# Kernel optimization log

Hardware: AMD Instinct MI355X
Metric: run time of the kernel (lower is better)

## Reference

```python
import jax, jax.numpy as jnp
import numpy as np

NUM_BANDS = 30
NUM_CH = 128
DIFF_HEAD_DIM = NUM_CH // 4 // 2  # 16
GRAPH_HEADS = 4
GRAPH_HD = NUM_CH // GRAPH_HEADS  # 32
SCALES = [2, 4, 8, 16, 32]


def _band_config():
    widths = np.array([2,3,3,3,3,3,3,3,3,3,3,8,8,8,8,8,8,8,8,8,8,8,8,16,16,16,16,16,16,16,17], dtype=np.float64)
    starts = np.concatenate([[0.0], np.cumsum(widths)])[:NUM_BANDS]
    freqs = (starts + widths[:NUM_BANDS] / 2.0) * 31.25
    slot = {2: 0, 4: 1, 8: 2, 16: 3, 32: 4}
    scale_slots, init_w = [], []
    for f in freqs:
        if f < 500:
            sc, iw = [8, 16, 32], [0.1, 0.3, 0.6]
        elif f < 2000:
            sc, iw = [4, 8, 16], [0.3, 0.4, 0.3]
        else:
            sc, iw = [2, 4, 8], [0.6, 0.3, 0.1]
        scale_slots.append([slot[s] for s in sc])
        init_w.append(iw)
    return freqs, np.array(scale_slots, np.int32), np.array(init_w, np.float32)

BAND_FREQS, SCALE_SLOTS, INIT_W = _band_config()


def setup_inputs() -> dict:
    key = jax.random.key(0)
    ks = iter(jax.random.split(key, 64))
    B, N, T, K = 4, NUM_CH, 512, NUM_BANDS

    def nrm(shape, fan):
        return jax.random.normal(next(ks), shape, jnp.float32) / np.sqrt(fan)

    inp = {}
    inp['x'] = jax.random.normal(next(ks), (B, N, T, K), jnp.float32)
    # per-band differential attention weights (stored [in, out])
    inp['Wq'] = nrm((K, N, N), N)
    inp['Wk'] = nrm((K, N, N), N)
    inp['Wv'] = nrm((K, N, N // 2), N)
    inp['Wo'] = nrm((K, N // 2, N), N // 2)
    inp['bo'] = jnp.zeros((K, N), jnp.float32)
    # per-band lambda predictors
    inp['lw1'] = nrm((K, 8, 16), 8)
    inp['lb1'] = jnp.zeros((K, 16), jnp.float32)
    inp['lw2'] = nrm((K, 16, 1), 16)
    inp['lb2'] = jnp.zeros((K, 1), jnp.float32)
    # shared multiscale conv kernels (torch OIH layout)
    for s in SCALES:
        inp[f'cw{s}'] = nrm((N, N, s), N * s)
        inp[f'cb{s}'] = jnp.zeros((N,), jnp.float32)
    inp['fusion_w'] = jnp.asarray(INIT_W)
    inp['band_embed'] = jnp.log(jnp.asarray(BAND_FREQS, jnp.float32) + 1.0)[:, None] * jax.random.normal(next(ks), (K, 64), jnp.float32) * 0.1
    # graph attention weights
    inp['gWq'] = nrm((N, N), N); inp['gbq'] = jnp.zeros((N,), jnp.float32)
    inp['gWk'] = nrm((N, N), N); inp['gbk'] = jnp.zeros((N,), jnp.float32)
    inp['gWv'] = nrm((N, N), N); inp['gbv'] = jnp.zeros((N,), jnp.float32)
    inp['gWo'] = nrm((N, N), N); inp['gbo'] = jnp.zeros((N,), jnp.float32)
    return inp


def reference(x, Wq, Wk, Wv, Wo, bo, lw1, lb1, lw2, lb2,
              cw2, cb2, cw4, cb4, cw8, cb8, cw16, cb16, cw32, cb32,
              fusion_w, band_embed, gWq, gbq, gWk, gbk, gWv, gbv, gWo, gbo):
    B, N, T, K = x.shape

    # ---- 1. Differential band attention (vectorized over the 30 bands) ----
    xb = jnp.transpose(x, (3, 0, 2, 1))                         # [K,B,T,N]
    q = jnp.einsum('kbtn,knm->kbtm', xb, Wq)
    kk = jnp.einsum('kbtn,knm->kbtm', xb, Wk)
    v = jnp.einsum('kbtn,knd->kbtd', xb, Wv)                    # [K,B,T,N/2]
    q1, q2 = jnp.split(q, 2, axis=-1)
    k1, k2 = jnp.split(kk, 2, axis=-1)
    inv = 1.0 / np.sqrt(DIFF_HEAD_DIM)
    a1 = jax.nn.softmax(jnp.einsum('kbtd,kbsd->kbts', q1, k1) * inv, axis=-1)
    a2 = jax.nn.softmax(jnp.einsum('kbtd,kbsd->kbts', q2, k2) * inv, axis=-1)

    def stats(a):  # mean / unbiased std / max / min over the [T,T] map
        return (a.mean(axis=(-2, -1)), jnp.std(a, axis=(-2, -1), ddof=1),
                a.max(axis=(-2, -1)), a.min(axis=(-2, -1)))

    st = jnp.stack(stats(a1) + stats(a2), axis=-1)              # [K,B,8]
    h = jax.nn.relu(jnp.einsum('kbi,kio->kbo', st, lw1) + lb1[:, None, :])
    lam = jax.nn.sigmoid(jnp.einsum('kbo,koj->kbj', h, lw2) + lb2[:, None, :])[..., None]  # [K,B,1,1]
    ad = a1 - lam * a2
    ob = jnp.einsum('kbts,kbsd->kbtd', ad, v)
    ob = jnp.einsum('kbtd,kdn->kbtn', ob, Wo) + bo[:, None, None, :]
    h1 = jnp.transpose(ob, (1, 3, 2, 0))                        # [B,N,T,K]

    # ---- 2. Frequency-adaptive multiscale conv fusion ----
    xm = jnp.transpose(h1, (0, 3, 1, 2)).reshape(B * K, N, T)   # bands into batch

    def conv(xc, w, b, s):
        y = jax.lax.conv_general_dilated(xc, w, (1,), [(s // 2, s // 2)],
                                         dimension_numbers=('NCH', 'OIH', 'NCH'))
        return y[:, :, :T] + b[None, :, None]                   # trim even-kernel extra frame

    co = jnp.stack([conv(xm, w, b, s) for (w, b, s) in
                    [(cw2, cb2, 2), (cw4, cb4, 4), (cw8, cb8, 8), (cw16, cb16, 16), (cw32, cb32, 32)]], 0)
    sw = jax.nn.softmax(fusion_w, axis=-1)                      # [K,3]
    Wfull = jnp.zeros((K, 5), x.dtype).at[jnp.arange(K)[:, None], jnp.asarray(SCALE_SLOTS)].set(sw)
    co = co.reshape(5, B, K, N, T)
    h2 = jnp.transpose(jnp.einsum('ks,sbknt->bknt', Wfull, co), (0, 2, 3, 1))  # [B,N,T,K]

    # ---- 3. Learnable harmonic graph attention across bands ----
    e = band_embed / (jnp.linalg.norm(band_embed, axis=-1, keepdims=True) + 1e-8)
    sim = e @ e.T
    vals, idx = jax.lax.top_k(sim, 5)
    A = jnp.zeros((K, K), x.dtype).at[jnp.arange(K)[:, None], idx].set(vals)
    A = (A + A.T) / 2
    M = B * T
    xg = jnp.transpose(h2, (0, 2, 3, 1)).reshape(M, K, N)       # [B*T, 30, 128]
    qg = jnp.transpose((xg @ gWq + gbq).reshape(M, K, GRAPH_HEADS, GRAPH_HD), (0, 2, 1, 3))
    kg = jnp.transpose((xg @ gWk + gbk).reshape(M, K, GRAPH_HEADS, GRAPH_HD), (0, 2, 1, 3))
    vg = jnp.transpose((xg @ gWv + gbv).reshape(M, K, GRAPH_HEADS, GRAPH_HD), (0, 2, 1, 3))
    sc = jnp.einsum('mhid,mhjd->mhij', qg, kg) / np.sqrt(float(GRAPH_HD))
    sc = jnp.where((A != 0)[None, None], sc, -jnp.inf)
    at = jnp.nan_to_num(jax.nn.softmax(sc, axis=-1))
    og = jnp.einsum('mhij,mhjd->mhid', at, vg)
    og = jnp.transpose(og, (0, 2, 1, 3)).reshape(M, K, N) @ gWo + gbo
    out = jnp.transpose(og.reshape(B, T, K, N), (0, 3, 1, 2))   # [B,N,T,K]
    return out
```

## Files before the change

kernel.cpp:

```cpp
#include <hip/hip_runtime.h>

typedef const float* fp;
typedef unsigned short u16;
typedef __attribute__((ext_vector_type(8))) short bf16x8;
typedef __attribute__((ext_vector_type(4))) float f32x4;

__device__ __forceinline__ u16 f2b(float f) {
  union { float f; unsigned u; } a; a.f = f;
  unsigned u = a.u;
  u += 0x7fffu + ((u >> 16) & 1u);
  return (u16)(u >> 16);
}
__device__ __forceinline__ void splitf(float x, u16& h, u16& l) {
  union { float f; unsigned u; } a; a.f = x;
  unsigned hu = a.u & 0xFFFF0000u;
  h = (u16)(hu >> 16);
  union { unsigned u; float f; } b; b.u = hu;
  l = f2b(x - b.f);
}

__global__ __launch_bounds__(64) void k_adj(fp be, float* mask) {
  __shared__ float e[30][65];
  __shared__ float sim[30][33];
  __shared__ float A[30][33];
  int tid = threadIdx.x;
  for (int idx = tid; idx < 30 * 64; idx += 64) e[idx / 64][idx % 64] = be[idx];
  __syncthreads();
  if (tid < 30) {
    float s = 0.f;
    for (int d = 0; d < 64; d++) s += e[tid][d] * e[tid][d];
    float sc = 1.0f / (sqrtf(s) + 1e-8f);
    for (int d = 0; d < 64; d++) e[tid][d] *= sc;
  }
  __syncthreads();
  if (tid < 30) {
    for (int j = 0; j < 30; j++) {
      float s = 0.f;
      for (int d = 0; d < 64; d++) s += e[tid][d] * e[j][d];
      sim[tid][j] = s;
    }
    for (int j = 0; j < 30; j++) A[tid][j] = 0.f;
  }
  __syncthreads();
  if (tid < 30) {
    unsigned used = 0;
    for (int t = 0; t < 5; t++) {
      float best = -1e30f; int bi = 0;
      for (int j = 0; j < 30; j++)
        if (!((used >> j) & 1u) && sim[tid][j] > best) { best = sim[tid][j]; bi = j; }
      A[tid][bi] = best; used |= 1u << bi;
    }
  }
  __syncthreads();
  for (int idx = tid; idx < 900; idx += 64) {
    int i = idx / 30, j = idx % 30;
    float s = A[i][j] + A[j][i];
    mask[idx] = (s != 0.0f) ? 1.0f : 0.0f;
  }
}

__global__ __launch_bounds__(256) void k_wt_band(fp Wq, fp Wk, fp Wv, u16* wh, u16* wl) {
  int kb = blockIdx.x, which = blockIdx.y;
  __shared__ float wsb[128][129];
  int tid = threadIdx.x;
  int M = (which == 2) ? 64 : 128;
  int sh = (which == 2) ? 6 : 7;
  fp src = (which == 0) ? (Wq + kb * 16384) : (which == 1) ? (Wk + kb * 16384) : (Wv + kb * 8192);
  for (int i = tid; i < 128 * M; i += 256) {
    int n = i >> sh, m = i & (M - 1);
    wsb[n][m] = src[i];
  }
  __syncthreads();
  long base = (long)kb * 40960 + which * 16384;
  for (int o = tid; o < 128 * M; o += 256) {
    int m = o >> 7, n = o & 127;
    u16 h, l; splitf(wsb[n][m], h, l);
    wh[base + m * 128 + n] = h; wl[base + m * 128 + n] = l;
  }
}

__global__ __launch_bounds__(256) void k_wt_graph(fp gWq, fp gWk, fp gWv, fp gWo,
                                                  u16* wh, u16* wl) {
  int w = blockIdx.x;
  fp src = (w == 0) ? gWq : (w == 1) ? gWk : (w == 2) ? gWv : gWo;
  __shared__ float wsb[128][129];
  int tid = threadIdx.x;
  for (int i = tid; i < 16384; i += 256) wsb[i >> 7][i & 127] = src[i];
  __syncthreads();
  long base = (long)w * 16384;
  for (int o = tid; o < 16384; o += 256) {
    int m = o >> 7, n = o & 127;
    u16 h, l; splitf(wsb[n][m], h, l);
    wh[base + m * 128 + n] = h; wl[base + m * 128 + n] = l;
  }
}

__global__ __launch_bounds__(256) void k_qkv(fp x, const u16* wh, const u16* wl,
                                             u16* qh, u16* ql, u16* kh, u16* kl,
                                             u16* vTh, u16* vTl) {
  int kb = blockIdx.z, b = blockIdx.y, t0 = blockIdx.x * 64;
  int tid = threadIdx.x;
  int wave = tid >> 6, lane = tid & 63, l15 = lane & 15, quad = lane >> 4;
  __shared__ u16 xs_h[64 * 136];
  __shared__ u16 xs_l[64 * 136];
  for (int i = tid; i < 8192; i += 256) {
    int tl = i >> 7, n = i & 127;
    float v = x[((long)(b * 128 + n) * 512 + t0 + tl) * 30 + kb];
    u16 h, l; splitf(v, h, l);
    xs_h[tl * 136 + n] = h; xs_l[tl * 136 + n] = l;
  }
  __syncthreads();
  int arow = wave * 16 + l15;
  bf16x8 Ah[4], Al[4];
#pragma unroll
  for (int kc = 0; kc < 4; kc++) {
    Ah[kc] = *(const bf16x8*)(xs_h + arow * 136 + kc * 32 + quad * 8);
    Al[kc] = *(const bf16x8*)(xs_l + arow * 136 + kc * 32 + quad * 8);
  }
  int pair = kb * 4 + b;
  const u16* wbh = wh + (long)kb * 40960;
  const u16* wbl = wl + (long)kb * 40960;
  for (int c = 0; c < 20; c++) {
    f32x4 d = {0.f, 0.f, 0.f, 0.f};
#pragma unroll
    for (int kc = 0; kc < 4; kc++) {
      long boff = (long)(c * 16 + l15) * 128 + kc * 32 + quad * 8;
      bf16x8 Bh = *(const bf16x8*)(wbh + boff);
      bf16x8 Bl = *(const bf16x8*)(wbl + boff);
      d = __builtin_amdgcn_mfma_f32_16x16x32_bf16(Ah[kc], Bh, d, 0, 0, 0);
      d = __builtin_amdgcn_mfma_f32_16x16x32_bf16(Ah[kc], Bl, d, 0, 0, 0);
      d = __builtin_amdgcn_mfma_f32_16x16x32_bf16(Al[kc], Bh, d, 0, 0, 0);
    }
    if (c < 8) {
      int m = c * 16 + l15;
#pragma unroll
      for (int r = 0; r < 4; r++) {
        int trow = t0 + wave * 16 + quad * 4 + r;
        u16 h, l; splitf(d[r], h, l);
        long o = ((long)pair * 512 + trow) * 128 + m;
        qh[o] = h; ql[o] = l;
      }
    } else if (c < 16) {
      int m = (c - 8) * 16 + l15;
#pragma unroll
      for (int r = 0; r < 4; r++) {
        int trow = t0 + wave * 16 + quad * 4 + r;
        u16 h, l; splitf(d[r], h, l);
        long o = ((long)pair * 512 + trow) * 128 + m;
        kh[o] = h; kl[o] = l;
      }
    } else {
      int dcol = (c - 16) * 16 + l15;
#pragma unroll
      for (int r = 0; r < 4; r++) {
        int trow = t0 + wave * 16 + quad * 4 + r;
        u16 h, l; splitf(d[r], h, l);
        long o = ((long)pair * 64 + dcol) * 512 + trow;
        vTh[o] = h; vTl[o] = l;
      }
    }
  }
}

__global__ __launch_bounds__(256) void k_flash(const u16* qh, const u16* ql,
                                               const u16* kh, const u16* kl,
                                               const u16* vTh, const u16* vTl,
                                               float* rowstats, float* ob1, float* ob2) {
  int pair = blockIdx.y;
  int t0 = blockIdx.x * 16;
  int tid = threadIdx.x;
  int wave = tid >> 6, lane = tid & 63;
  int l15 = lane & 15, quad = lane >> 4;

  __shared__ float fbig[8704];
  __shared__ float st[2][16][4][4];
  __shared__ float fin[2][16][2];

  const long pb = (long)pair * 512 * 128;
  const u16* qhb = qh + pb; const u16* qlb = ql + pb;
  const u16* khb = kh + pb; const u16* klb = kl + pb;

  float sc[2][8][4];
  float mw[2][4];
#pragma unroll
  for (int h = 0; h < 2; h++) {
    long abase = (long)(t0 + l15) * 128 + h * 64 + quad * 8;
    bf16x8 Ah0 = *(const bf16x8*)(qhb + abase);
    bf16x8 Ah1 = *(const bf16x8*)(qhb + abase + 32);
    bf16x8 Al0 = *(const bf16x8*)(qlb + abase);
    bf16x8 Al1 = *(const bf16x8*)(qlb + abase + 32);
#pragma unroll
    for (int ct = 0; ct < 8; ct++) {
      int scol = wave * 128 + ct * 16 + l15;
      long bbase = (long)scol * 128 + h * 64 + quad * 8;
      bf16x8 Bh0 = *(const bf16x8*)(khb + bbase);
      bf16x8 Bh1 = *(const bf16x8*)(khb + bbase + 32);
      bf16x8 Bl0 = *(const bf16x8*)(klb + bbase);
      bf16x8 Bl1 = *(const bf16x8*)(klb + bbase + 32);
      f32x4 d = {0.f, 0.f, 0.f, 0.f};
      d = __builtin_amdgcn_mfma_f32_16x16x32_bf16(Ah0, Bh0, d, 0, 0, 0);
      d = __builtin_amdgcn_mfma_f32_16x16x32_bf16(Ah1, Bh1, d, 0, 0, 0);
      d = __builtin_amdgcn_mfma_f32_16x16x32_bf16(Ah0, Bl0, d, 0, 0, 0);
      d = __builtin_amdgcn_mfma_f32_16x16x32_bf16(Ah1, Bl1, d, 0, 0, 0);
      d = __builtin_amdgcn_mfma_f32_16x16x32_bf16(Al0, Bh0, d, 0, 0, 0);
      d = __builtin_amdgcn_mfma_f32_16x16x32_bf16(Al1, Bh1, d, 0, 0, 0);
#pragma unroll
      for (int r = 0; r < 4; r++) sc[h][ct][r] = d[r] * 0.25f;
    }
  }
#pragma unroll
  for (int h = 0; h < 2; h++)
#pragma unroll
    for (int r = 0; r < 4; r++) {
      float m = -1e30f, mnv = 1e30f;
#pragma unroll
      for (int ct = 0; ct < 8; ct++) { m = fmaxf(m, sc[h][ct][r]); mnv = fminf(mnv, sc[h][ct][r]); }
      for (int d = 1; d < 16; d <<= 1) { m = fmaxf(m, __shfl_xor(m, d)); mnv = fminf(mnv, __shfl_xor(mnv, d)); }
      float z = 0.f, s2 = 0.f;
#pragma unroll
      for (int ct = 0; ct < 8; ct++) {
        float e = expf(sc[h][ct][r] - m); z += e; s2 += e * e;
        sc[h][ct][r] = e;
      }
      for (int d = 1; d < 16; d <<= 1) { z += __shfl_xor(z, d); s2 += __shfl_xor(s2, d); }
      mw[h][r] = m;
      if (l15 == 0) {
        st[h][quad * 4 + r][wave][0] = m;  st[h][quad * 4 + r][wave][1] = z;
        st[h][quad * 4 + r][wave][2] = s2; st[h][quad * 4 + r][wave][3] = mnv;
      }
    }
  __syncthreads();
  if (tid < 32) {
    int row = tid & 15, h = tid >> 4;
    float Mf = -1e30f, mnf = 1e30f;
    for (int w = 0; w < 4; w++) { Mf = fmaxf(Mf, st[h][row][w][0]); mnf = fminf(mnf, st[h][row][w][3]); }
    float Z = 0.f, S2 = 0.f;
    for (int w = 0; w < 4; w++) {
      float f = expf(st[h][row][w][0] - Mf);
      Z += st[h][row][w][1] * f; S2 += st[h][row][w][2] * f * f;
    }
    float* o = rowstats + ((long)pair * 512 + t0 + row) * 8 + h * 4;
    o[0] = Mf; o[1] = Z; o[2] = S2; o[3] = mnf;
    fin[h][row][0] = Mf; fin[h][row][1] = 1.0f / Z;
  }
  __syncthreads();
  u16* pbuf = (u16*)fbig;
#pragma unroll
  for (int h = 0; h < 2; h++)
#pragma unroll
    for (int r = 0; r < 4; r++) {
      int row = quad * 4 + r;
      float scale = expf(mw[h][r] - fin[h][row][0]) * fin[h][row][1];
#pragma unroll
      for (int ct = 0; ct < 8; ct++) {
        float p = sc[h][ct][r] * scale;
        pbuf[((h * 4 + wave) * 16 + row) * 136 + ct * 16 + l15] = f2b(p);
      }
    }
  __syncthreads();
  f32x4 acc[2][4];
#pragma unroll
  for (int h = 0; h < 2; h++)
#pragma unroll
    for (int nt = 0; nt < 4; nt++) acc[h][nt] = {0.f, 0.f, 0.f, 0.f};
  const u16* vThb = vTh + (long)pair * 64 * 512;
  const u16* vTlb = vTl + (long)pair * 64 * 512;
#pragma unroll
  for (int kc = 0; kc < 4; kc++) {
    int sbase = wave * 128 + kc * 32 + quad * 8;
    bf16x8 A0 = *(const bf16x8*)(pbuf + ((0 * 4 + wave) * 16 + l15) * 136 + kc * 32 + quad * 8);
    bf16x8 A1 = *(const bf16x8*)(pbuf + ((1 * 4 + wave) * 16 + l15) * 136 + kc * 32 + quad * 8);
#pragma unroll
    for (int nt = 0; nt < 4; nt++) {
      long vo = (long)(nt * 16 + l15) * 512 + sbase;
      bf16x8 Vh = *(const bf16x8*)(vThb + vo);
      bf16x8 Vl = *(const bf16x8*)(vTlb + vo);
      acc[0][nt] = __builtin_amdgcn_mfma_f32_16x16x32_bf16(A0, Vh, acc[0][nt], 0, 0, 0);
      acc[0][nt] = __builtin_amdgcn_mfma_f32_16x16x32_bf16(A0, Vl, acc[0][nt], 0, 0, 0);
      acc[1][nt] = __builtin_amdgcn_mfma_f32_16x16x32_bf16(A1, Vh, acc[1][nt], 0, 0, 0);
      acc[1][nt] = __builtin_amdgcn_mfma_f32_16x16x32_bf16(A1, Vl, acc[1][nt], 0, 0, 0);
    }
  }
  __syncthreads();
  float* obr = fbig;
#pragma unroll
  for (int h = 0; h < 2; h++)
#pragma unroll
    for (int nt = 0; nt < 4; nt++)
#pragma unroll
      for (int r = 0; r < 4; r++)
        obr[((wave * 2 + h) * 16 + quad * 4 + r) * 68 + nt * 16 + l15] = acc[h][nt][r];
  __syncthreads();
  for (int i = tid; i < 2048; i += 256) {
    int h = i >> 10, row = (i >> 6) & 15, d = i & 63;
    float s = 0.f;
    for (int w = 0; w < 4; w++) s += obr[((w * 2 + h) * 16 + row) * 68 + d];
    float* dst = (h == 0 ? ob1 : ob2);
    dst[((long)pair * 512 + t0 + row) * 64 + d] = s;
  }
}

__global__ __launch_bounds__(64) void k_lam(const float* rowstats, fp lw1, fp lb1,
                                            fp lw2, fp lb2, float* lam) {
  int pair = blockIdx.x; int kb = pair >> 2;
  int tid = threadIdx.x;
  const float* rs = rowstats + (long)pair * 512 * 8;
  float mx1 = -1e30f, mn1 = 1e30f, ss1 = 0.f, mx2 = -1e30f, mn2 = 1e30f, ss2 = 0.f;
  for (int j = 0; j < 8; j++) {
    const float* rr = rs + (long)(j * 64 + tid) * 8;
    float M1 = rr[0], Z1 = rr[1], S21 = rr[2], m1 = rr[3];
    float M2 = rr[4], Z2 = rr[5], S22 = rr[6], m2 = rr[7];
    mx1 = fmaxf(mx1, 1.0f / Z1); mn1 = fminf(mn1, expf(m1 - M1) / Z1); ss1 += S21 / (Z1 * Z1);
    mx2 = fmaxf(mx2, 1.0f / Z2); mn2 = fminf(mn2, expf(m2 - M2) / Z2); ss2 += S22 / (Z2 * Z2);
  }
  __shared__ float red[64][8];
  red[tid][0] = mx1; red[tid][1] = mn1; red[tid][2] = ss1;
  red[tid][3] = mx2; red[tid][4] = mn2; red[tid][5] = ss2;
  __syncthreads();
  if (tid == 0) {
    for (int e = 1; e < 64; e++) {
      mx1 = fmaxf(mx1, red[e][0]); mn1 = fminf(mn1, red[e][1]); ss1 += red[e][2];
      mx2 = fmaxf(mx2, red[e][3]); mn2 = fminf(mn2, red[e][4]); ss2 += red[e][5];
    }
    const float mean = 1.0f / 512.0f;
    const float n = 262144.0f;
    float v1 = (ss1 - n * mean * mean) / (n - 1.0f); float sd1 = sqrtf(fmaxf(v1, 0.f));
    float v2 = (ss2 - n * mean * mean) / (n - 1.0f); float sd2 = sqrtf(fmaxf(v2, 0.f));
    float stv[8] = { mean, sd1, mx1, mn1, mean, sd2, mx2, mn2 };
    float acc = lb2[kb];
    for (int o = 0; o < 16; o++) {
      float h = lb1[kb * 16 + o];
      for (int i = 0; i < 8; i++) h += stv[i] * lw1[(kb * 8 + i) * 16 + o];
      h = fmaxf(h, 0.f);
      acc += h * lw2[kb * 16 + o];
    }
    lam[pair] = 1.0f / (1.0f + expf(-acc));
  }
}

__global__ __launch_bounds__(128) void k_ep(const float* ob1, const float* ob2,
                                            const float* lam, fp Wo, fp bo, float* h1) {
  int pair = blockIdx.y; int kb = pair >> 2, b = pair & 3;
  int t0 = blockIdx.x * 8;
  int tid = threadIdx.x;
  float lv = lam[pair];
  __shared__ float obs[8][68];
  for (int i = tid; i < 512; i += 128) {
    int r = i >> 6, d = i & 63;
    long o = ((long)pair * 512 + t0 + r) * 64 + d;
    obs[r][d] = ob1[o] - lv * ob2[o];
  }
  __syncthreads();
  int n = tid;
  float acc[8];
#pragma unroll
  for (int r = 0; r < 8; r++) acc[r] = bo[kb * 128 + n];
  for (int dd = 0; dd < 64; dd++) {
    float w = Wo[(kb * 64 + dd) * 128 + n];
#pragma unroll
    for (int r = 0; r < 8; r++) acc[r] += obs[r][dd] * w;
  }
#pragma unroll
  for (int r = 0; r < 8; r++)
    h1[((long)(b * 30 + kb) * 512 + t0 + r) * 128 + n] = acc[r];
}

__global__ __launch_bounds__(256) void k_ck(fp fw, fp cw2, fp cw4, fp cw8,
                                            fp cw16, fp cw32, u16* ckh, u16* ckl) {
  long idx = (long)blockIdx.x * 256 + threadIdx.x;
  int ni = idx & 127;
  int no = (idx >> 7) & 127;
  int g  = (int)(idx >> 14);
  int kb, r;
  if (g < 192)      { kb = g >> 5;                r = g & 31; }
  else if (g < 336) { int gg = g - 192; kb = 6 + (gg >> 4);  r = 8 + (gg & 15); }
  else              { int gg = g - 336; kb = 15 + (gg >> 3); r = 12 + (gg & 7); }
  float f0 = fw[kb * 3 + 0], f1 = fw[kb * 3 + 1], f2 = fw[kb * 3 + 2];
  float mx = fmaxf(f0, fmaxf(f1, f2));
  float e0 = expf(f0 - mx), e1 = expf(f1 - mx), e2 = expf(f2 - mx);
  float zi = 1.0f / (e0 + e1 + e2);
  float sw[3] = { e0 * zi, e1 * zi, e2 * zi };
  int sbase; fp cws[3];
  if (kb < 6)       { sbase = 8; cws[0] = cw8;  cws[1] = cw16; cws[2] = cw32; }
  else if (kb < 15) { sbase = 4; cws[0] = cw4;  cws[1] = cw8;  cws[2] = cw16; }
  else              { sbase = 2; cws[0] = cw2;  cws[1] = cw4;  cws[2] = cw8;  }
  float val = 0.f;
  int rs = r - 16;
#pragma unroll
  for (int j = 0; j < 3; j++) {
    int s = sbase << j;
    int tau = rs + (s >> 1);
    if (tau >= 0 && tau < s) val += sw[j] * cws[j][((long)no * 128 + ni) * s + tau];
  }
  u16 h, l; splitf(val, h, l);
  ckh[idx] = h; ckl[idx] = l;
}

__global__ __launch_bounds__(256) void k_conv(const float* h1, const u16* ckh,
                                              const u16* ckl, fp fw,
                                              fp cb2, fp cb4, fp cb8, fp cb16,
                                              fp cb32, u16* h2h, u16* h2l) {
  int kb = blockIdx.z, b = blockIdx.y, t0 = blockIdx.x * 64;
  int tid = threadIdx.x;
  int wave = tid >> 6, lane = tid & 63, l15 = lane & 15, quad = lane >> 4;
  __shared__ u16 xs_h[96 * 136];
  __shared__ u16 xs_l[96 * 136];
  const float* xrow = h1 + (long)(b * 30 + kb) * 512 * 128;
  for (int i = tid; i < 3072; i += 256) {
    int row = i >> 5, c4 = (i & 31) << 2;
    int t = t0 - 16 + row;
    float4 xv = {0.f, 0.f, 0.f, 0.f};
    if (t >= 0 && t < 512) xv = *(const float4*)(xrow + (long)t * 128 + c4);
    u16 h, l;
    splitf(xv.x, h, l); xs_h[row * 136 + c4 + 0] = h; xs_l[row * 136 + c4 + 0] = l;
    splitf(xv.y, h, l); xs_h[row * 136 + c4 + 1] = h; xs_l[row * 136 + c4 + 1] = l;
    splitf(xv.z, h, l); xs_h[row * 136 + c4 + 2] = h; xs_l[row * 136 + c4 + 2] = l;
    splitf(xv.w, h, l); xs_h[row * 136 + c4 + 3] = h; xs_l[row * 136 + c4 + 3] = l;
  }
  float f0 = fw[kb * 3 + 0], f1 = fw[kb * 3 + 1], f2 = fw[kb * 3 + 2];
  float mx = fmaxf(f0, fmaxf(f1, f2));
  float e0 = expf(f0 - mx), e1 = expf(f1 - mx), e2 = expf(f2 - mx);
  float zi = 1.0f / (e0 + e1 + e2);
  float sw0 = e0 * zi, sw1 = e1 * zi, sw2 = e2 * zi;
  int rlo, rhi, gbase; fp c0, c1, c2;
  if (kb < 6)       { rlo = 0;  rhi = 32; gbase = kb * 32;            c0 = cb8; c1 = cb16; c2 = cb32; }
  else if (kb < 15) { rlo = 8;  rhi = 24; gbase = 192 + (kb - 6) * 16;  c0 = cb4; c1 = cb8;  c2 = cb16; }
  else              { rlo = 12; rhi = 20; gbase = 336 + (kb - 15) * 8;  c0 = cb2; c1 = cb4;  c2 = cb8;  }
  __syncthreads();
  f32x4 acc[4][2];
#pragma unroll
  for (int mt = 0; mt < 4; mt++) { acc[mt][0] = {0.f,0.f,0.f,0.f}; acc[mt][1] = {0.f,0.f,0.f,0.f}; }
  for (int r = rlo; r < rhi; r++) {
    const u16* wh = ckh + ((long)(gbase + r - rlo) * 128 + wave * 32 + l15) * 128;
    const u16* wl = ckl + ((long)(gbase + r - rlo) * 128 + wave * 32 + l15) * 128;
#pragma unroll
    for (int c = 0; c < 4; c++) {
      int koff = c * 32 + quad * 8;
      bf16x8 Bh0 = *(const bf16x8*)(wh + koff);
      bf16x8 Bh1 = *(const bf16x8*)(wh + 2048 + koff);
      bf16x8 Bl0 = *(const bf16x8*)(wl + koff);
      bf16x8 Bl1 = *(const bf16x8*)(wl + 2048 + koff);
#pragma unroll
      for (int mt = 0; mt < 4; mt++) {
        int arow = mt * 16 + l15 + r;
        bf16x8 Ah = *(const bf16x8*)(xs_h + arow * 136 + koff);
        bf16x8 Al = *(const bf16x8*)(xs_l + arow * 136 + koff);
        acc[mt][0] = __builtin_amdgcn_mfma_f32_16x16x32_bf16(Ah, Bh0, acc[mt][0], 0, 0, 0);
        acc[mt][0] = __builtin_amdgcn_mfma_f32_16x16x32_bf16(Ah, Bl0, acc[mt][0], 0, 0, 0);
        acc[mt][0] = __builtin_amdgcn_mfma_f32_16x16x32_bf16(Al, Bh0, acc[mt][0], 0, 0, 0);
        acc[mt][1] = __builtin_amdgcn_mfma_f32_16x16x32_bf16(Ah, Bh1, acc[mt][1], 0, 0, 0);
        acc[mt][1] = __builtin_amdgcn_mfma_f32_16x16x32_bf16(Ah, Bl1, acc[mt][1], 0, 0, 0);
        acc[mt][1] = __builtin_amdgcn_mfma_f32_16x16x32_bf16(Al, Bh1, acc[mt][1], 0, 0, 0);
      }
    }
  }
  int no0 = wave * 32 + l15;
  float bias0 = sw0 * c0[no0] + sw1 * c1[no0] + sw2 * c2[no0];
  float bias1 = sw0 * c0[no0 + 16] + sw1 * c1[no0 + 16] + sw2 * c2[no0 + 16];
#pragma unroll
  for (int mt = 0; mt < 4; mt++)
#pragma unroll
    for (int reg = 0; reg < 4; reg++) {
      int t = t0 + mt * 16 + quad * 4 + reg;
      long ob = ((long)(b * 512 + t) * 30 + kb) * 128 + no0;
      u16 h, l;
      splitf(acc[mt][0][reg] + bias0, h, l); h2h[ob] = h;      h2l[ob] = l;
      splitf(acc[mt][1][reg] + bias1, h, l); h2h[ob + 16] = h; h2l[ob + 16] = l;
    }
}

__global__ __launch_bounds__(256) void k_gattn(const u16* h2h, const u16* h2l,
                                               const u16* gwh, const u16* gwl,
                                               const float* maskw,
                                               fp gbq, fp gbk, fp gbv, fp gbo,
                                               float* out) {
  int m = blockIdx.x; int b = m >> 9; int t = m & 511;
  int tid = threadIdx.x;
  int wave = tid >> 6, lane = tid & 63, l15 = lane & 15, quad = lane >> 4;
  __shared__ float qs[32][136];
  __shared__ float ks[32][136];
  __shared__ float vs[32][136];
  u16* ogs_h = (u16*)&qs[0][0];
  u16* ogs_l = ogs_h + 32 * 136;

  {
    int mtile = wave & 1;
    int c0 = (wave >> 1) * 12;
    long abase0 = (long)m * 30 * 128;
    bf16x8 Ah[4], Al[4];
    bf16x8 zero8 = {0, 0, 0, 0, 0, 0, 0, 0};
    int row = mtile * 16 + l15;
#pragma unroll
    for (int kc = 0; kc < 4; kc++) {
      if (row < 30) {
        Ah[kc] = *(const bf16x8*)(h2h + abase0 + (long)row * 128 + kc * 32 + quad * 8);
        Al[kc] = *(const bf16x8*)(h2l + abase0 + (long)row * 128 + kc * 32 + quad * 8);
      } else { Ah[kc] = zero8; Al[kc] = zero8; }
    }
    for (int cc = 0; cc < 12; cc++) {
      int c = c0 + cc;
      f32x4 d = {0.f, 0.f, 0.f, 0.f};
#pragma unroll
      for (int kc = 0; kc < 4; kc++) {
        long boff = (long)(c * 16 + l15) * 128 + kc * 32 + quad * 8;
        bf16x8 Bh = *(const bf16x8*)(gwh + boff);
        bf16x8 Bl = *(const bf16x8*)(gwl + boff);
        d = __builtin_amdgcn_mfma_f32_16x16x32_bf16(Ah[kc], Bh, d, 0, 0, 0);
        d = __builtin_amdgcn_mfma_f32_16x16x32_bf16(Ah[kc], Bl, d, 0, 0, 0);
        d = __builtin_amdgcn_mfma_f32_16x16x32_bf16(Al[kc], Bh, d, 0, 0, 0);
      }
      int region = c >> 3;
      int ch = (c & 7) * 16 + l15;
      float bias = (region == 0) ? gbq[ch] : (region == 1) ? gbk[ch] : gbv[ch];
      float (*dst)[136] = (region == 0) ? qs : (region == 1) ? ks : vs;
#pragma unroll
      for (int r = 0; r < 4; r++) {
        int rowo = mtile * 16 + quad * 4 + r;
        if (rowo < 30) dst[rowo][ch] = d[r] + bias;
      }
    }
  }
  __syncthreads();

  float p[30]; float iZ = 0.f; int hi = 0, ii = 0;
  if (tid < 120) {
    hi = tid / 30; ii = tid % 30;
    int hb = hi * 32;
    float4 qv[8];
#pragma unroll
    for (int dq = 0; dq < 8; dq++) qv[dq] = *(const float4*)&qs[ii][hb + dq * 4];
    float mx = -1e30f;
#pragma unroll
    for (int j = 0; j < 30; j++) {
      float s = 0.f;
      const float4* kr = (const float4*)&ks[j][hb];
#pragma unroll
      for (int dq = 0; dq < 8; dq++) {
        float4 kv = kr[dq];
        s += qv[dq].x * kv.x + qv[dq].y * kv.y + qv[dq].z * kv.z + qv[dq].w * kv.w;
      }
      s *= 0.17677669529663687f;
      p[j] = (maskw[ii * 30 + j] != 0.f) ? s : -1e30f;
      mx = fmaxf(mx, p[j]);
    }
    float Z = 0.f;
#pragma unroll
    for (int j = 0; j < 30; j++) { float e = expf(p[j] - mx); p[j] = e; Z += e; }
    iZ = 1.0f / Z;
  }
  __syncthreads();
  if (tid < 120) {
    int hb = hi * 32;
#pragma unroll
    for (int dq = 0; dq < 8; dq++) {
      float sx = 0.f, sy = 0.f, sz = 0.f, sw2 = 0.f;
#pragma unroll
      for (int j = 0; j < 30; j++) {
        float4 vv = *(const float4*)&vs[j][hb + dq * 4];
        sx += p[j] * vv.x; sy += p[j] * vv.y; sz += p[j] * vv.z; sw2 += p[j] * vv.w;
      }
      float o4[4] = { sx * iZ, sy * iZ, sz * iZ, sw2 * iZ };
#pragma unroll
      for (int cpt = 0; cpt < 4; cpt++) {
        u16 h, l; splitf(o4[cpt], h, l);
        ogs_h[ii * 136 + hb + dq * 4 + cpt] = h;
        ogs_l[ii * 136 + hb + dq * 4 + cpt] = l;
      }
    }
  }
  __syncthreads();

  {
    int mtile = wave & 1;
    int nc0 = (wave >> 1) * 4;
    int row = mtile * 16 + l15;
    bf16x8 Ah[4], Al[4];
#pragma unroll
    for (int kc = 0; kc < 4; kc++) {
      Ah[kc] = *(const bf16x8*)(ogs_h + row * 136 + kc * 32 + quad * 8);
      Al[kc] = *(const bf16x8*)(ogs_l + row * 136 + kc * 32 + quad * 8);
    }
    for (int cc = 0; cc < 4; cc++) {
      int nchunk = nc0 + cc;
      f32x4 d = {0.f, 0.f, 0.f, 0.f};
#pragma unroll
      for (int kc = 0; kc < 4; kc++) {
        long boff = (long)(384 + nchunk * 16 + l15) * 128 + kc * 32 + quad * 8;
        bf16x8 Bh = *(const bf16x8*)(gwh + boff);
        bf16x8 Bl = *(const bf16x8*)(gwl + boff);
        d = __builtin_amdgcn_mfma_f32_16x16x32_bf16(Ah[kc], Bh, d, 0, 0, 0);
        d = __builtin_amdgcn_mfma_f32_16x16x32_bf16(Ah[kc], Bl, d, 0, 0, 0);
        d = __builtin_amdgcn_mfma_f32_16x16x32_bf16(Al[kc], Bh, d, 0, 0, 0);
      }
      int n = nchunk * 16 + l15;
      float gb = gbo[n];
      long obase = ((long)(b * 128 + n) * 512 + t) * 30;
#pragma unroll
      for (int r = 0; r < 4; r++) {
        int kbo = mtile * 16 + quad * 4 + r;
        if (kbo < 30) out[obase + kbo] = d[r] + gb;
      }
    }
  }
}

extern "C" void kernel_launch(void* const* d_in, const int* in_sizes, int n_in,
                              void* d_out, int out_size, void* d_ws, size_t ws_size,
                              hipStream_t stream) {
  fp x = (fp)d_in[0], Wq = (fp)d_in[1], Wk = (fp)d_in[2], Wv = (fp)d_in[3],
     Wo = (fp)d_in[4], bo = (fp)d_in[5], lw1 = (fp)d_in[6], lb1 = (fp)d_in[7],
     lw2 = (fp)d_in[8], lb2 = (fp)d_in[9],
     cw2 = (fp)d_in[10], cb2 = (fp)d_in[11], cw4 = (fp)d_in[12], cb4 = (fp)d_in[13],
     cw8 = (fp)d_in[14], cb8 = (fp)d_in[15], cw16 = (fp)d_in[16], cb16 = (fp)d_in[17],
     cw32 = (fp)d_in[18], cb32 = (fp)d_in[19], fw = (fp)d_in[20], be = (fp)d_in[21],
     gWq = (fp)d_in[22], gbq = (fp)d_in[23], gWk = (fp)d_in[24], gbk = (fp)d_in[25],
     gWv = (fp)d_in[26], gbv = (fp)d_in[27], gWo = (fp)d_in[28], gbo = (fp)d_in[29];
  (void)in_sizes; (void)n_in; (void)out_size; (void)ws_size;

  float* ws = (float*)d_ws;
  u16* qh  = (u16*)ws;
  u16* ql  = (u16*)(ws + 3932160L);
  u16* kh  = (u16*)(ws + 7864320L);
  u16* kl  = (u16*)(ws + 11796480L);
  u16* vTh = (u16*)(ws + 15728640L);
  u16* vTl = (u16*)(ws + 17694720L);
  float* rowstats = ws + 19660800L;
  float* lam      = ws + 20152320L;
  u16* wqkT_h = (u16*)(ws + 20152448L);
  u16* wqkT_l = (u16*)(ws + 20766848L);
  u16* gwT_h  = (u16*)(ws + 21381248L);
  u16* gwT_l  = (u16*)(ws + 21414016L);
  float* maskw = ws + 21446784L;
  float* ob1 = ws + 21447808L;
  float* ob2 = ws + 25379968L;
  float* h1  = ws;
  u16* h2h = (u16*)(ws + 7864320L);
  u16* h2l = (u16*)(ws + 11796480L);
  u16* ckh = (u16*)(ws + 21447808L);
  u16* ckl = (u16*)(ws + 25183360L);

  k_adj<<<1, 64, 0, stream>>>(be, maskw);
  k_wt_band<<<dim3(30, 3), 256, 0, stream>>>(Wq, Wk, Wv, wqkT_h, wqkT_l);
  k_wt_graph<<<4, 256, 0, stream>>>(gWq, gWk, gWv, gWo, gwT_h, gwT_l);
  k_qkv<<<dim3(8, 4, 30), 256, 0, stream>>>(x, wqkT_h, wqkT_l, qh, ql, kh, kl, vTh, vTl);
  k_flash<<<dim3(32, 120), 256, 0, stream>>>(qh, ql, kh, kl, vTh, vTl, rowstats, ob1, ob2);
  k_lam<<<120, 64, 0, stream>>>(rowstats, lw1, lb1, lw2, lb2, lam);
  k_ep<<<dim3(64, 120), 128, 0, stream>>>(ob1, ob2, lam, Wo, bo, h1);
  k_ck<<<29184, 256, 0, stream>>>(fw, cw2, cw4, cw8, cw16, cw32, ckh, ckl);
  k_conv<<<dim3(8, 4, 30), 256, 0, stream>>>(h1, ckh, ckl, fw, cb2, cb4, cb8, cb16, cb32, h2h, h2l);
  k_gattn<<<2048, 256, 0, stream>>>(h2h, h2l, gwT_h, gwT_l, maskw, gbq, gbk, gbv, gbo, (float*)d_out);
}
```

Measured before the change: 882.1 us.

## Move output projection to split-bf16 MFMA and pre-split intermediates for conv

The differential-attention epilogue becomes an MFMA GEMM with a pre-transposed, hi/lo-split Wo, prepared in an extra k_wt_band slice, replacing the scalar FMA loop. The flash kernel now emits ob1/ob2 as hi/lo bf16 pairs, and the epilogue emits h1 the same way, so k_conv loads bf16x8 vectors directly instead of splitting floats. Flash recomputes exp in the P pass rather than keeping exp values in registers, which may lower register pressure. Grid orders for flash and conv are linearized to change block scheduling and L2 locality. Accuracy rests on the 3-term split-bf16 product, and the conv grid launches idle blocks for padded band slots.

New measurement: 1.105 ms. 1.25x slower.

```diff
diff --git a/kernel.cpp b/kernel.cpp
--- a/kernel.cpp
+++ b/kernel.cpp
@@ -59,10 +59,25 @@
   }
 }
 
-__global__ __launch_bounds__(256) void k_wt_band(fp Wq, fp Wk, fp Wv, u16* wh, u16* wl) {
+__global__ __launch_bounds__(256) void k_wt_band(fp Wq, fp Wk, fp Wv, fp Wo,
+                                                 u16* wh, u16* wl, u16* woh, u16* wol) {
   int kb = blockIdx.x, which = blockIdx.y;
   __shared__ float wsb[128][129];
   int tid = threadIdx.x;
+  if (which == 3) {
+    fp src = Wo + kb * 8192;
+    for (int i = tid; i < 8192; i += 256) {
+      int d = i >> 7, n = i & 127;
+      wsb[n][d] = src[i];
+    }
+    __syncthreads();
+    long base = (long)kb * 8192;
+    for (int o = tid; o < 8192; o += 256) {
+      u16 h, l; splitf(wsb[o >> 6][o & 63], h, l);
+      woh[base + o] = h; wol[base + o] = l;
+    }
+    return;
+  }
   int M = (which == 2) ? 64 : 128;
   int sh = (which == 2) ? 6 : 7;
   fp src = (which == 0) ? (Wq + kb * 16384) : (which == 1) ? (Wk + kb * 16384) : (Wv + kb * 8192);
@@ -165,9 +180,11 @@
 __global__ __launch_bounds__(256) void k_flash(const u16* qh, const u16* ql,
                                                const u16* kh, const u16* kl,
                                                const u16* vTh, const u16* vTl,
-                                               float* rowstats, float* ob1, float* ob2) {
-  int pair = blockIdx.y;
-  int t0 = blockIdx.x * 16;
+                                               float* rowstats,
+                                               u16* ob1h, u16* ob1l, u16* ob2h, u16* ob2l) {
+  int bid = blockIdx.x;
+  int pair = bid % 120;
+  int t0 = (bid / 120) * 16;
   int tid = threadIdx.x;
   int wave = tid >> 6, lane = tid & 63;
   int l15 = lane & 15, quad = lane >> 4;
@@ -181,7 +198,6 @@
   const u16* khb = kh + pb; const u16* klb = kl + pb;
 
   float sc[2][8][4];
-  float mw[2][4];
 #pragma unroll
   for (int h = 0; h < 2; h++) {
     long abase = (long)(t0 + l15) * 128 + h * 64 + quad * 8;
@@ -218,12 +234,8 @@
       for (int d = 1; d < 16; d <<= 1) { m = fmaxf(m, __shfl_xor(m, d)); mnv = fminf(mnv, __shfl_xor(mnv, d)); }
       float z = 0.f, s2 = 0.f;
 #pragma unroll
-      for (int ct = 0; ct < 8; ct++) {
-        float e = expf(sc[h][ct][r] - m); z += e; s2 += e * e;
-        sc[h][ct][r] = e;
-      }
+      for (int ct = 0; ct < 8; ct++) { float e = expf(sc[h][ct][r] - m); z += e; s2 += e * e; }
       for (int d = 1; d < 16; d <<= 1) { z += __shfl_xor(z, d); s2 += __shfl_xor(s2, d); }
-      mw[h][r] = m;
       if (l15 == 0) {
         st[h][quad * 4 + r][wave][0] = m;  st[h][quad * 4 + r][wave][1] = z;
         st[h][quad * 4 + r][wave][2] = s2; st[h][quad * 4 + r][wave][3] = mnv;
@@ -250,10 +262,10 @@
 #pragma unroll
     for (int r = 0; r < 4; r++) {
       int row = quad * 4 + r;
-      float scale = expf(mw[h][r] - fin[h][row][0]) * fin[h][row][1];
+      float Mf = fin[h][row][0], iZ = fin[h][row][1];
 #pragma unroll
       for (int ct = 0; ct < 8; ct++) {
-        float p = sc[h][ct][r] * scale;
+        float p = expf(sc[h][ct][r] - Mf) * iZ;
         pbuf[((h * 4 + wave) * 16 + row) * 136 + ct * 16 + l15] = f2b(p);
       }
     }
@@ -295,8 +307,10 @@
     int h = i >> 10, row = (i >> 6) & 15, d = i & 63;
     float s = 0.f;
     for (int w = 0; w < 4; w++) s += obr[((w * 2 + h) * 16 + row) * 68 + d];
-    float* dst = (h == 0 ? ob1 : ob2);
-    dst[((long)pair * 512 + t0 + row) * 64 + d] = s;
+    u16 hh, ll; splitf(s, hh, ll);
+    long o = ((long)pair * 512 + t0 + row) * 64 + d;
+    if (h == 0) { ob1h[o] = hh; ob1l[o] = ll; }
+    else        { ob2h[o] = hh; ob2l[o] = ll; }
   }
 }
 
@@ -338,31 +352,53 @@
   }
 }
 
-__global__ __launch_bounds__(128) void k_ep(const float* ob1, const float* ob2,
-                                            const float* lam, fp Wo, fp bo, float* h1) {
+__global__ __launch_bounds__(256) void k_ep(const u16* ob1h, const u16* ob1l,
+                                            const u16* ob2h, const u16* ob2l,
+                                            const float* lam, const u16* woh, const u16* wol,
+                                            fp bo, u16* h1h, u16* h1l) {
   int pair = blockIdx.y; int kb = pair >> 2, b = pair & 3;
-  int t0 = blockIdx.x * 8;
-  int tid = threadIdx.x;
+  int t0 = blockIdx.x * 16;
+  int tid = threadIdx.x;
+  int wave = tid >> 6, lane = tid & 63, l15 = lane & 15, quad = lane >> 4;
   float lv = lam[pair];
-  __shared__ float obs[8][68];
-  for (int i = tid; i < 512; i += 128) {
-    int r = i >> 6, d = i & 63;
-    long o = ((long)pair * 512 + t0 + r) * 64 + d;
-    obs[r][d] = ob1[o] - lv * ob2[o];
-  }
-  __syncthreads();
-  int n = tid;
-  float acc[8];
-#pragma unroll
-  for (int r = 0; r < 8; r++) acc[r] = bo[kb * 128 + n];
-  for (int dd = 0; dd < 64; dd++) {
-    float w = Wo[(kb * 64 + dd) * 128 + n];
-#pragma unroll
-    for (int r = 0; r < 8; r++) acc[r] += obs[r][dd] * w;
-  }
-#pragma unroll
-  for (int r = 0; r < 8; r++)
-    h1[((long)(b * 30 + kb) * 512 + t0 + r) * 128 + n] = acc[r];
+  long ab = ((long)pair * 512 + t0 + l15) * 64 + quad * 8;
+  bf16x8 A1h[2], A1l[2], A2h[2], A2l[2];
+#pragma unroll
+  for (int kc = 0; kc < 2; kc++) {
+    A1h[kc] = *(const bf16x8*)(ob1h + ab + kc * 32);
+    A1l[kc] = *(const bf16x8*)(ob1l + ab + kc * 32);
+    A2h[kc] = *(const bf16x8*)(ob2h + ab + kc * 32);
+    A2l[kc] = *(const bf16x8*)(ob2l + ab + kc * 32);
+  }
+  const u16* wbh = woh + (long)kb * 8192;
+  const u16* wbl = wol + (long)kb * 8192;
+#pragma unroll
+  for (int cc = 0; cc < 2; cc++) {
+    int c = wave * 2 + cc;
+    f32x4 d1 = {0.f, 0.f, 0.f, 0.f}, d2 = {0.f, 0.f, 0.f, 0.f};
+#pragma unroll
+    for (int kc = 0; kc < 2; kc++) {
+      long boff = (long)(c * 16 + l15) * 64 + kc * 32 + quad * 8;
+      bf16x8 Bh = *(const bf16x8*)(wbh + boff);
+      bf16x8 Bl = *(const bf16x8*)(wbl + boff);
+      d1 = __builtin_amdgcn_mfma_f32_16x16x32_bf16(A1h[kc], Bh, d1, 0, 0, 0);
+      d1 = __builtin_amdgcn_mfma_f32_16x16x32_bf16(A1h[kc], Bl, d1, 0, 0, 0);
+      d1 = __builtin_amdgcn_mfma_f32_16x16x32_bf16(A1l[kc], Bh, d1, 0, 0, 0);
+      d2 = __builtin_amdgcn_mfma_f32_16x16x32_bf16(A2h[kc], Bh, d2, 0, 0, 0);
+      d2 = __builtin_amdgcn_mfma_f32_16x16x32_bf16(A2h[kc], Bl, d2, 0, 0, 0);
+      d2 = __builtin_amdgcn_mfma_f32_16x16x32_bf16(A2l[kc], Bh, d2, 0, 0, 0);
+    }
+    int n = c * 16 + l15;
+    float bias = bo[kb * 128 + n];
+#pragma unroll
+    for (int r = 0; r < 4; r++) {
+      int t = t0 + quad * 4 + r;
+      float val = d1[r] - lv * d2[r] + bias;
+      u16 h, l; splitf(val, h, l);
+      long o = ((long)(b * 30 + kb) * 512 + t) * 128 + n;
+      h1h[o] = h; h1l[o] = l;
+    }
+  }
 }
 
 __global__ __launch_bounds__(256) void k_ck(fp fw, fp cw2, fp cw4, fp cw8,
@@ -396,26 +432,32 @@
   ckh[idx] = h; ckl[idx] = l;
 }
 
-__global__ __launch_bounds__(256) void k_conv(const float* h1, const u16* ckh,
-                                              const u16* ckl, fp fw,
+__global__ __launch_bounds__(256) void k_conv(const u16* h1h, const u16* h1l,
+                                              const u16* ckh, const u16* ckl, fp fw,
                                               fp cb2, fp cb4, fp cb8, fp cb16,
                                               fp cb32, u16* h2h, u16* h2l) {
-  int kb = blockIdx.z, b = blockIdx.y, t0 = blockIdx.x * 64;
+  int bid = blockIdx.x;
+  int kb = bid & 31;
+  if (kb >= 30) return;
+  int rem = bid >> 5;
+  int b = rem & 3, t0 = (rem >> 2) * 64;
   int tid = threadIdx.x;
   int wave = tid >> 6, lane = tid & 63, l15 = lane & 15, quad = lane >> 4;
   __shared__ u16 xs_h[96 * 136];
   __shared__ u16 xs_l[96 * 136];
-  const float* xrow = h1 + (long)(b * 30 + kb) * 512 * 128;
-  for (int i = tid; i < 3072; i += 256) {
-    int row = i >> 5, c4 = (i & 31) << 2;
+  const u16* xrh = h1h + (long)(b * 30 + kb) * 512 * 128;
+  const u16* xrl = h1l + (long)(b * 30 + kb) * 512 * 128;
+  bf16x8 zero8 = {0, 0, 0, 0, 0, 0, 0, 0};
+  for (int i = tid; i < 1536; i += 256) {
+    int row = i >> 4, c8 = (i & 15) << 3;
     int t = t0 - 16 + row;
-    float4 xv = {0.f, 0.f, 0.f, 0.f};
-    if (t >= 0 && t < 512) xv = *(const float4*)(xrow + (long)t * 128 + c4);
-    u16 h, l;
-    splitf(xv.x, h, l); xs_h[row * 136 + c4 + 0] = h; xs_l[row * 136 + c4 + 0] = l;
-    splitf(xv.y, h, l); xs_h[row * 136 + c4 + 1] = h; xs_l[row * 136 + c4 + 1] = l;
-    splitf(xv.z, h, l); xs_h[row * 136 + c4 + 2] = h; xs_l[row * 136 + c4 + 2] = l;
-    splitf(xv.w, h, l); xs_h[row * 136 + c4 + 3] = h; xs_l[row * 136 + c4 + 3] = l;
+    bf16x8 vh = zero8, vl = zero8;
+    if (t >= 0 && t < 512) {
+      vh = *(const bf16x8*)(xrh + (long)t * 128 + c8);
+      vl = *(const bf16x8*)(xrl + (long)t * 128 + c8);
+    }
+    *(bf16x8*)(xs_h + row * 136 + c8) = vh;
+    *(bf16x8*)(xs_l + row * 136 + c8) = vl;
   }
   float f0 = fw[kb * 3 + 0], f1 = fw[kb * 3 + 1], f2 = fw[kb * 3 + 2];
   float mx = fmaxf(f0, fmaxf(f1, f2));
@@ -423,9 +465,9 @@
   float zi = 1.0f / (e0 + e1 + e2);
   float sw0 = e0 * zi, sw1 = e1 * zi, sw2 = e2 * zi;
   int rlo, rhi, gbase; fp c0, c1, c2;
-  if (kb < 6)       { rlo = 0;  rhi = 32; gbase = kb * 32;            c0 = cb8; c1 = cb16; c2 = cb32; }
-  else if (kb < 15) { rlo = 8;  rhi = 24; gbase = 192 + (kb - 6) * 16;  c0 = cb4; c1 = cb8;  c2 = cb16; }
-  else              { rlo = 12; rhi = 20; gbase = 336 + (kb - 15) * 8;  c0 = cb2; c1 = cb4;  c2 = cb8;  }
+  if (kb < 6)       { rlo = 0;  rhi = 32; gbase = kb * 32;             c0 = cb8; c1 = cb16; c2 = cb32; }
+  else if (kb < 15) { rlo = 8;  rhi = 24; gbase = 192 + (kb - 6) * 16; c0 = cb4; c1 = cb8;  c2 = cb16; }
+  else              { rlo = 12; rhi = 20; gbase = 336 + (kb - 15) * 8; c0 = cb2; c1 = cb4;  c2 = cb8;  }
   __syncthreads();
   f32x4 acc[4][2];
 #pragma unroll
@@ -631,22 +673,27 @@
   u16* gwT_h  = (u16*)(ws + 21381248L);
   u16* gwT_l  = (u16*)(ws + 21414016L);
   float* maskw = ws + 21446784L;
-  float* ob1 = ws + 21447808L;
-  float* ob2 = ws + 25379968L;
-  float* h1  = ws;
+  u16* woT_h = (u16*)(ws + 21447808L);
+  u16* woT_l = (u16*)(ws + 21570688L);
+  u16* ob1h = (u16*)(ws + 21693568L);
+  u16* ob1l = (u16*)(ws + 23659648L);
+  u16* ob2h = (u16*)(ws + 25625728L);
+  u16* ob2l = (u16*)(ws + 27591808L);
+  u16* h1h = (u16*)ws;
+  u16* h1l = (u16*)(ws + 3932160L);
   u16* h2h = (u16*)(ws + 7864320L);
   u16* h2l = (u16*)(ws + 11796480L);
-  u16* ckh = (u16*)(ws + 21447808L);
-  u16* ckl = (u16*)(ws + 25183360L);
+  u16* ckh = (u16*)(ws + 21693568L);
+  u16* ckl = (u16*)(ws + 25429120L);
 
   k_adj<<<1, 64, 0, stream>>>(be, maskw);
-  k_wt_band<<<dim3(30, 3), 256, 0, stream>>>(Wq, Wk, Wv, wqkT_h, wqkT_l);
+  k_wt_band<<<dim3(30, 4), 256, 0, stream>>>(Wq, Wk, Wv, Wo, wqkT_h, wqkT_l, woT_h, woT_l);
   k_wt_graph<<<4, 256, 0, stream>>>(gWq, gWk, gWv, gWo, gwT_h, gwT_l);
   k_qkv<<<dim3(8, 4, 30), 256, 0, stream>>>(x, wqkT_h, wqkT_l, qh, ql, kh, kl, vTh, vTl);
-  k_flash<<<dim3(32, 120), 256, 0, stream>>>(qh, ql, kh, kl, vTh, vTl, rowstats, ob1, ob2);
+  k_flash<<<3840, 256, 0, stream>>>(qh, ql, kh, kl, vTh, vTl, rowstats, ob1h, ob1l, ob2h, ob2l);
   k_lam<<<120, 64, 0, stream>>>(rowstats, lw1, lb1, lw2, lb2, lam);
-  k_ep<<<dim3(64, 120), 128, 0, stream>>>(ob1, ob2, lam, Wo, bo, h1);
+  k_ep<<<dim3(32, 120), 256, 0, stream>>>(ob1h, ob1l, ob2h, ob2l, lam, woT_h, woT_l, bo, h1h, h1l);
   k_ck<<<29184, 256, 0, stream>>>(fw, cw2, cw4, cw8, cw16, cw32, ckh, ckl);
-  k_conv<<<dim3(8, 4, 30), 256, 0, stream>>>(h1, ckh, ckl, fw, cb2, cb4, cb8, cb16, cb32, h2h, h2l);
+  k_conv<<<1024, 256, 0, stream>>>(h1h, h1l, ckh, ckl, fw, cb2, cb4, cb8, cb16, cb32, h2h, h2l);
   k_gattn<<<2048, 256, 0, stream>>>(h2h, h2l, gwT_h, gwT_l, maskw, gbq, gbk, gbv, gbo, (float*)d_out);
 }
```
